# Kernel optimization log

Hardware: AMD Instinct MI355X
Metric: run time of the kernel (lower is better)

Reference implementation:

```python
import jax, jax.numpy as jnp
import numpy as np

B, N, K, IN = 8, 2048, 8, 5
BN = B * N

def _lin(k, i, o):
    s = 1.0 / np.sqrt(i)
    return jax.random.uniform(k, (i, o), jnp.float32, -s, s)

def setup_inputs() -> dict:
    key = jax.random.key(0)
    ks = jax.random.split(key, 12)
    inp = {"points": jax.random.normal(ks[0], (B, N, IN), jnp.float32)}
    dims = [(IN * 2, 64), (64 * 2, 128), (128 * 2, 256)]
    for n, (i, o) in enumerate(dims, 1):
        inp[f"W{n}"] = _lin(ks[n], i, o)
        inp[f"b{n}"] = jnp.zeros((o,), jnp.float32)
        inp[f"g{n}"] = jnp.ones((o,), jnp.float32)
        inp[f"be{n}"] = jnp.zeros((o,), jnp.float32)
    inp["Wf1"] = _lin(ks[10], 448, 512); inp["bf1"] = jnp.zeros((512,), jnp.float32)
    inp["gf"] = jnp.ones((512,), jnp.float32); inp["bef"] = jnp.zeros((512,), jnp.float32)
    inp["Wf2"] = _lin(ks[11], 512, 128); inp["bf2"] = jnp.zeros((128,), jnp.float32)
    return inp

def _lrelu(x):
    return jnp.where(x >= 0, x, 0.2 * x)

def _bn(x, g, b, eps=1e-5):
    # BatchNorm1d in training mode: per-feature batch statistics
    m = x.mean(0)
    v = x.var(0)
    return (x - m) * jax.lax.rsqrt(v + eps) * g + b

def _knn_idx(pos):
    # pos: [B,N,3] -> neighbor indices [B,N,K], self excluded
    sq = (pos * pos).sum(-1)
    d = sq[:, :, None] + sq[:, None, :] - 2.0 * jnp.einsum('bnc,bmc->bnm', pos, pos)
    d = d + jnp.eye(N, dtype=d.dtype) * 1e10  # exclude self
    _, idx = jax.lax.top_k(-d, K)
    return idx

def _edge_conv(x, src, dst, W, b, g, be):
    # PyG EdgeConv: msg = nn(cat[x_i, x_j - x_i]); aggr='max' at target i
    xc = x[dst]
    xn = x[src]
    h = jnp.concatenate([xc, xn - xc], axis=-1) @ W + b
    h = _bn(_lrelu(h), g, be)
    return jax.ops.segment_max(h, dst, num_segments=BN)

def reference(points, W1, b1, g1, be1, W2, b2, g2, be2, W3, b3, g3, be3,
              Wf1, bf1, gf, bef, Wf2, bf2):
    pos = points[..., :3]                      # [B,N,3]
    idx = _knn_idx(pos)                        # [B,N,K]
    offs = (jnp.arange(B) * N)[:, None, None]
    src = (idx + offs).reshape(-1)             # neighbor (source) node ids [E]
    dst = jnp.repeat(jnp.arange(BN), K)        # center (target) node ids [E]
    x = points.reshape(BN, IN)
    x1 = _edge_conv(x, src, dst, W1, b1, g1, be1)   # [BN,64]
    x2 = _edge_conv(x1, src, dst, W2, b2, g2, be2)  # [BN,128]
    x3 = _edge_conv(x2, src, dst, W3, b3, g3, be3)  # [BN,256]
    xs = jnp.concatenate([x1, x2, x3], axis=-1).reshape(B, N, 448)
    gfeat = xs.max(axis=1)                     # global max pool per cloud [B,448]
    h = _bn(_lrelu(gfeat @ Wf1 + bf1), gf, bef)
    return h @ Wf2 + bf2                       # [B,128]
```

## Files before the change

kernel.cpp:

```cpp
#include <hip/hip_runtime.h>
#include <math.h>

#define B_ 8
#define N_ 2048
#define K_ 8
#define IN_ 5
#define BN_ (B_*N_)
#define NEDGE_ (BN_*K_)
#define GRP 8
#define SEG_ 32
#define CSEG_ (N_/SEG_)
#define CHUNKS_ (N_/GRP)

typedef unsigned short ushort8_ __attribute__((ext_vector_type(8)));
typedef short bf16x8_ __attribute__((ext_vector_type(8)));
typedef float f32x4_ __attribute__((ext_vector_type(4)));

__device__ inline unsigned short f2bf(float f) {
    unsigned int u = __float_as_uint(f);
    u += 0x7fffu + ((u >> 16) & 1u);
    return (unsigned short)(u >> 16);
}
__device__ inline float bf2f(unsigned short h) {
    return __uint_as_float(((unsigned int)h) << 16);
}

__global__ __launch_bounds__(256) void knn_part(const float4* __restrict__ P4,
                                                unsigned long long* __restrict__ part) {
    int tid = threadIdx.x;
    int bblk = blockIdx.x >> 3;
    int q = blockIdx.x * 256 + tid;
    int nloc = q & (N_-1);
    int seg = blockIdx.y;

    float4 qp = P4[q];
    float qx2 = -2.0f*qp.x, qy2 = -2.0f*qp.y, qz2 = -2.0f*qp.z;
    float qsq = qp.w;

    unsigned int bd[K_], bi[K_];
#pragma unroll
    for (int k = 0; k < K_; ++k) { bd[k] = 0xFFFFFFFFu; bi[k] = 0xFFFFFFFFu; }

    const float4* __restrict__ cb = P4 + ((size_t)bblk << 11) + (size_t)seg*CSEG_;
    int jbase = seg * CSEG_;

#pragma unroll 8
    for (int jj = 0; jj < CSEG_; ++jj) {
        float4 c = cb[jj];
        float d = qsq + c.w;
        d = fmaf(qx2, c.x, d);
        d = fmaf(qy2, c.y, d);
        d = fmaf(qz2, c.z, d);
        unsigned int cd = __float_as_uint(d);
        int jg = jbase + jj;
        cd = (jg == nloc) ? 0xFFFFFFFFu : cd;
        unsigned int ci = (unsigned int)jg;
#pragma unroll
        for (int p = 0; p < K_; ++p) {
            bool lt = cd < bd[p];
            unsigned int nd = lt ? cd : bd[p];
            unsigned int xd = lt ? bd[p] : cd;
            unsigned int ni = lt ? ci : bi[p];
            unsigned int xi = lt ? bi[p] : ci;
            bd[p] = nd; cd = xd; bi[p] = ni; ci = xi;
        }
    }
    unsigned long long* op = part + ((size_t)seg * BN_ + q) * K_;
#pragma unroll
    for (int k = 0; k < K_; ++k)
        op[k] = ((unsigned long long)bd[k] << 32) | bi[k];
}

__global__ __launch_bounds__(128) void knn_merge(const unsigned long long* __restrict__ part,
                                                 int* __restrict__ src) {
    int q = blockIdx.x * 128 + threadIdx.x;
    int b = q / N_;
    unsigned long long best[K_];
#pragma unroll
    for (int k = 0; k < K_; ++k) best[k] = ~0ull;
    for (int s = 0; s < SEG_; ++s) {
        const unsigned long long* lp = part + ((size_t)s * BN_ + q) * K_;
#pragma unroll
        for (int k = 0; k < K_; ++k) {
            unsigned long long key = lp[k];
            if (key >= best[K_-1]) break;
            unsigned long long cur = key;
#pragma unroll
            for (int p = 0; p < K_; ++p) {
                unsigned long long lo = best[p] < cur ? best[p] : cur;
                unsigned long long hi = best[p] < cur ? cur : best[p];
                best[p] = lo; cur = hi;
            }
        }
    }
#pragma unroll
    for (int k = 0; k < K_; ++k)
        src[(size_t)q*K_ + k] = b*N_ + (int)(best[k] & 0xFFFFFFFFu);
}

__global__ __launch_bounds__(256) void cast_prep1(const float* __restrict__ X,
                                                  unsigned short* __restrict__ Xh,
                                                  unsigned short* __restrict__ Xl,
                                                  float4* __restrict__ P4,
                                                  const float* __restrict__ W1,
                                                  const float* __restrict__ b1,
                                                  unsigned short* __restrict__ WTh,
                                                  unsigned short* __restrict__ WTl,
                                                  float* __restrict__ cvec) {
    const int total8 = BN_ * 32 / 8;
    int t = blockIdx.x * 256 + threadIdx.x;
    if (t < total8) {
        int m = t >> 2;
        int k0 = (t & 3) * 8;
        ushort8_ vh, vl;
#pragma unroll
        for (int j = 0; j < 8; ++j) {
            int k = k0 + j;
            float v = (k < IN_) ? X[(size_t)m*IN_ + k] : 0.0f;
            unsigned short h = f2bf(v);
            vh[j] = h;
            vl[j] = f2bf(v - bf2f(h));
        }
        *(ushort8_*)(Xh + (size_t)m*32 + k0) = vh;
        *(ushort8_*)(Xl + (size_t)m*32 + k0) = vl;
        if (t < BN_) {
            const float* p = X + (size_t)t*IN_;
            float x = p[0], y = p[1], z = p[2];
            P4[t] = make_float4(x, y, z, x*x + y*y + z*z);
        }
    } else {
        int idx = t - total8;
        const int nWT = 2*64*32;
        if (idx < nWT) {
            int n = idx >> 5;
            int k = idx & 31;
            float val = 0.0f;
            if (k < IN_) {
                if (n < 64) val = W1[(size_t)k*64 + n] - W1[(size_t)(IN_+k)*64 + n];
                else        val = W1[(size_t)(IN_+k)*64 + (n - 64)];
            }
            unsigned short h = f2bf(val);
            WTh[(size_t)n*32 + k] = h;
            WTl[(size_t)n*32 + k] = f2bf(val - bf2f(h));
        } else if (idx < nWT + 64) {
            int c = idx - nWT;
            cvec[c] = b1[c];
        }
    }
}

__global__ __launch_bounds__(256) void prep_layer(const float* __restrict__ W,
                                                  const float* __restrict__ scale,
                                                  const float* __restrict__ shift,
                                                  const float* __restrict__ bias,
                                                  unsigned short* __restrict__ WTh,
                                                  unsigned short* __restrict__ WTl,
                                                  float* __restrict__ cvec,
                                                  int Cin, int C, int Kpad) {
    int idx = blockIdx.x * 256 + threadIdx.x;
    int nWT = 2*C*Kpad;
    if (idx < nWT) {
        int n = idx / Kpad;
        int k = idx % Kpad;
        float val = 0.0f;
        if (k < Cin) {
            float s = scale[k];
            if (n < C) val = s * (W[(size_t)k*C + n] - W[(size_t)(Cin+k)*C + n]);
            else       val = s * W[(size_t)(Cin+k)*C + (n - C)];
        }
        unsigned short h = f2bf(val);
        WTh[(size_t)n*Kpad + k] = h;
        WTl[(size_t)n*Kpad + k] = f2bf(val - bf2f(h));
    } else if (idx < nWT + C) {
        int c = idx - nWT;
        float acc = bias[c];
        for (int d = 0; d < Cin; ++d) acc += shift[d] * W[(size_t)d*C + c];
        cvec[c] = acc;
    }
}

__global__ __launch_bounds__(256) void mfma_dual(const unsigned short* __restrict__ Xh,
                                                 const unsigned short* __restrict__ Xl,
                                                 const unsigned short* __restrict__ WTh,
                                                 const unsigned short* __restrict__ WTl,
                                                 float* __restrict__ PQ, int K, int Ntot,
                                                 int gx) {
    __shared__ unsigned short sXh[128*32], sXl[128*32], sWh[128*32], sWl[128*32];
    int n = blockIdx.x;
    int by = (n & 7) + 8*(n/(8*gx));
    int bx = (n >> 3) % gx;
    int tid = threadIdx.x, l = tid & 63, w = tid >> 6;
    int wr = w >> 1, wc = w & 1;
    int bm = by * 128, bn0 = bx * 128;

    f32x4_ acc[4][4];
#pragma unroll
    for (int i = 0; i < 4; ++i)
#pragma unroll
        for (int j = 0; j < 4; ++j) acc[i][j] = (f32x4_){0.f, 0.f, 0.f, 0.f};

    for (int k0 = 0; k0 < K; k0 += 32) {
#pragma unroll
        for (int i = 0; i < 2; ++i) {
            int idx = tid + i*256;
            int row = idx >> 2;
            int col0 = (idx & 3) * 8;
            size_t gxo = (size_t)(bm  + row)*K + k0 + col0;
            size_t gwo = (size_t)(bn0 + row)*K + k0 + col0;
            int lo_ = ((row << 6) | (col0 << 1)) ^ ((row & 7) << 4);
            *(ushort8_*)((char*)sXh + lo_) = *(const ushort8_*)(Xh + gxo);
            *(ushort8_*)((char*)sXl + lo_) = *(const ushort8_*)(Xl + gxo);
            *(ushort8_*)((char*)sWh + lo_) = *(const ushort8_*)(WTh + gwo);
            *(ushort8_*)((char*)sWl + lo_) = *(const ushort8_*)(WTl + gwo);
        }
        __syncthreads();

        int kb = (l >> 4) << 4;
        bf16x8_ bh[4], bl4[4];
#pragma unroll
        for (int nf = 0; nf < 4; ++nf) {
            int rn = wc*64 + nf*16 + (l & 15);
            int o = ((rn << 6) | kb) ^ ((rn & 7) << 4);
            bh[nf]  = *(const bf16x8_*)((const char*)sWh + o);
            bl4[nf] = *(const bf16x8_*)((const char*)sWl + o);
        }
#pragma unroll
        for (int mf = 0; mf < 4; ++mf) {
            int rm = wr*64 + mf*16 + (l & 15);
            int o = ((rm << 6) | kb) ^ ((rm & 7) << 4);
            bf16x8_ ah = *(const bf16x8_*)((const char*)sXh + o);
            bf16x8_ al = *(const bf16x8_*)((const char*)sXl + o);
#pragma unroll
            for (int nf = 0; nf < 4; ++nf) {
                acc[mf][nf] = __builtin_amdgcn_mfma_f32_16x16x32_bf16(ah, bh[nf],  acc[mf][nf], 0, 0, 0);
                acc[mf][nf] = __builtin_amdgcn_mfma_f32_16x16x32_bf16(ah, bl4[nf], acc[mf][nf], 0, 0, 0);
                acc[mf][nf] = __builtin_amdgcn_mfma_f32_16x16x32_bf16(al, bh[nf],  acc[mf][nf], 0, 0, 0);
            }
        }
        __syncthreads();
    }

    int r0 = (l >> 4) << 2, cB = l & 15;
#pragma unroll
    for (int mf = 0; mf < 4; ++mf)
#pragma unroll
        for (int nf = 0; nf < 4; ++nf) {
            int col = bn0 + wc*64 + nf*16 + cB;
#pragma unroll
            for (int reg = 0; reg < 4; ++reg) {
                int row = bm + wr*64 + mf*16 + r0 + reg;
                PQ[(size_t)row*Ntot + col] = acc[mf][nf][reg];
            }
        }
}

__global__ void combine_kernel(const float* __restrict__ P, const float* __restrict__ Q,
                               const float* __restrict__ cvec, const int* __restrict__ src,
                               unsigned short* __restrict__ Xh_out, unsigned short* __restrict__ Xl_out,
                               float* __restrict__ partial, float* __restrict__ gpart,
                               int C, int S) {
    int pb = blockIdx.x;
    int lb = (pb & 7) * CHUNKS_ + (pb >> 3);
    int c = threadIdx.x;
    int i0 = lb * GRP;
    float cv = cvec[c];
    float sum = 0.f, ssq = 0.f;
    float bmx = -INFINITY;
    for (int g = 0; g < GRP; ++g) {
        int i = i0 + g;
        float p = P[(size_t)i*S + c] + cv;
        float mx = -INFINITY;
#pragma unroll
        for (int k = 0; k < K_; ++k) {
            int s = src[(size_t)i*K_ + k];
            float h = p + Q[(size_t)s*S + c];
            float l = (h >= 0.f) ? h : 0.2f*h;
            sum += l; ssq += l*l;
            mx = fmaxf(mx, l);
        }
        if (Xh_out) {
            unsigned short hh = f2bf(mx);
            Xh_out[(size_t)i*C + c] = hh;
            Xl_out[(size_t)i*C + c] = f2bf(mx - bf2f(hh));
        }
        bmx = fmaxf(bmx, mx);
    }
    gpart[(size_t)lb*C + c] = bmx;
    partial[(size_t)lb*2*C + c]     = sum;
    partial[(size_t)lb*2*C + C + c] = ssq;
}

__global__ __launch_bounds__(256) void reduce_kernel(const float* __restrict__ partial, int nblocks, int C,
                              const float* __restrict__ g, const float* __restrict__ be,
                              float* __restrict__ scale, float* __restrict__ shift) {
    int c = blockIdx.x;
    float s0 = 0.f, s1 = 0.f;
    for (int blk = threadIdx.x; blk < nblocks; blk += 256) {
        s0 += partial[(size_t)blk*2*C + c];
        s1 += partial[(size_t)blk*2*C + C + c];
    }
    __shared__ float l0[256], l1[256];
    l0[threadIdx.x] = s0; l1[threadIdx.x] = s1;
    __syncthreads();
    for (int off = 128; off > 0; off >>= 1) {
        if (threadIdx.x < off) {
            l0[threadIdx.x] += l0[threadIdx.x + off];
            l1[threadIdx.x] += l1[threadIdx.x + off];
        }
        __syncthreads();
    }
    if (threadIdx.x == 0) {
        float mean = l0[0] / (float)NEDGE_;
        float var  = l1[0] / (float)NEDGE_ - mean*mean;
        float sc = g[c] * rsqrtf(var + 1e-5f);
        scale[c] = sc;
        shift[c] = be[c] - mean*sc;
    }
}

__global__ __launch_bounds__(1024) void gmax_finalize(
        const float* __restrict__ gp1, const float* __restrict__ gp2, const float* __restrict__ gp3,
        const float* __restrict__ sc1, const float* __restrict__ sh1,
        const float* __restrict__ sc2, const float* __restrict__ sh2,
        const float* __restrict__ sc3, const float* __restrict__ sh3,
        float* __restrict__ gfeat) {
    int b = blockIdx.x, grp = blockIdx.y;
    const float *gp, *sc, *sh; int C, c0, coff;
    if (grp == 0)      { gp = gp1; sc = sc1; sh = sh1; C = 64;  c0 = 0;            coff = 0;   }
    else if (grp <= 2) { gp = gp2; sc = sc2; sh = sh2; C = 128; c0 = (grp-1)*64;   coff = 64;  }
    else               { gp = gp3; sc = sc3; sh = sh3; C = 256; c0 = (grp-3)*64;   coff = 192; }
    int cl = threadIdx.x & 63;
    int stripe = threadIdx.x >> 6;
    int c = c0 + cl;
    float mx = -INFINITY;
    for (int ch = stripe; ch < CHUNKS_; ch += 16)
        mx = fmaxf(mx, gp[((size_t)b*CHUNKS_ + ch)*C + c]);
    __shared__ float red[16][64];
    red[stripe][cl] = mx;
    __syncthreads();
    for (int off = 8; off > 0; off >>= 1) {
        if (stripe < off) red[stripe][cl] = fmaxf(red[stripe][cl], red[stripe+off][cl]);
        __syncthreads();
    }
    if (stripe == 0)
        gfeat[b*448 + coff + c] = sc[c]*red[0][cl] + sh[c];
}

__global__ __launch_bounds__(256) void final1(const float* __restrict__ gfeat,
                                              const float* __restrict__ Wf1, const float* __restrict__ bf1,
                                              const float* __restrict__ gf, const float* __restrict__ bef,
                                              float* __restrict__ H) {
    __shared__ float gfs[B_][448];
    __shared__ float red[4][64][B_];
    int t = threadIdx.x;
    int cl = t & 63;
    int stripe = t >> 6;
    int c = blockIdx.x * 64 + cl;
    for (int e = t; e < B_*448; e += 256) gfs[e/448][e%448] = gfeat[e];
    __syncthreads();
    float acc[B_] = {};
    for (int d = stripe*112; d < stripe*112 + 112; ++d) {
        float w = Wf1[(size_t)d*512 + c];
#pragma unroll
        for (int r = 0; r < B_; ++r) acc[r] += gfs[r][d] * w;
    }
#pragma unroll
    for (int r = 0; r < B_; ++r) red[stripe][cl][r] = acc[r];
    __syncthreads();
    if (stripe == 0) {
        float v[B_];
        float b1v = bf1[c];
#pragma unroll
        for (int r = 0; r < B_; ++r) {
            float a = red[0][cl][r] + red[1][cl][r] + red[2][cl][r] + red[3][cl][r] + b1v;
            v[r] = (a >= 0.f) ? a : 0.2f*a;
        }
        float mean = 0.f;
#pragma unroll
        for (int r = 0; r < B_; ++r) mean += v[r];
        mean *= (1.0f/B_);
        float var = 0.f;
#pragma unroll
        for (int r = 0; r < B_; ++r) { float dd = v[r] - mean; var += dd*dd; }
        var *= (1.0f/B_);
        float sc = gf[c] * rsqrtf(var + 1e-5f);
        float sh = bef[c] - mean*sc;
#pragma unroll
        for (int r = 0; r < B_; ++r) H[(size_t)r*512 + c] = v[r]*sc + sh;
    }
}

__global__ __launch_bounds__(128) void final2(const float* __restrict__ H,
                                              const float* __restrict__ Wf2, const float* __restrict__ bf2,
                                              float* __restrict__ out) {
    int b = blockIdx.x, c = threadIdx.x;
    __shared__ float hs[512];
    for (int e = c; e < 512; e += 128) hs[e] = H[(size_t)b*512 + e];
    __syncthreads();
    float a = bf2[c];
    for (int d = 0; d < 512; ++d) a += hs[d] * Wf2[(size_t)d*128 + c];
    out[b*128 + c] = a;
}

extern "C" void kernel_launch(void* const* d_in, const int* in_sizes, int n_in,
                              void* d_out, int out_size, void* d_ws, size_t ws_size,
                              hipStream_t stream) {
    (void)in_sizes; (void)n_in; (void)out_size; (void)ws_size;
    const float* points = (const float*)d_in[0];
    const float* W1 = (const float*)d_in[1];  const float* b1 = (const float*)d_in[2];
    const float* g1 = (const float*)d_in[3];  const float* be1 = (const float*)d_in[4];
    const float* W2 = (const float*)d_in[5];  const float* b2 = (const float*)d_in[6];
    const float* g2 = (const float*)d_in[7];  const float* be2 = (const float*)d_in[8];
    const float* W3 = (const float*)d_in[9];  const float* b3 = (const float*)d_in[10];
    const float* g3 = (const float*)d_in[11]; const float* be3 = (const float*)d_in[12];
    const float* Wf1 = (const float*)d_in[13]; const float* bf1 = (const float*)d_in[14];
    const float* gf = (const float*)d_in[15];  const float* bef = (const float*)d_in[16];
    const float* Wf2 = (const float*)d_in[17]; const float* bf2 = (const float*)d_in[18];
    float* out = (float*)d_out;

    size_t off = 0;
    char* base = (char*)d_ws;
    auto carve = [&](size_t bytes) -> void* {
        void* p = base + off;
        off += (bytes + 255) & ~(size_t)255;
        return p;
    };
    int*   src     = (int*)  carve((size_t)NEDGE_ * 4);
    float* PQ      = (float*)carve((size_t)BN_ * 512 * 4);
    float* gp1     = (float*)carve((size_t)(BN_/GRP) * 64 * 4);
    float* gp2     = (float*)carve((size_t)(BN_/GRP) * 128 * 4);
    float* gp3     = (float*)carve((size_t)(BN_/GRP) * 256 * 4);
    unsigned short* XhA = (unsigned short*)carve((size_t)BN_ * 128 * 2);
    unsigned short* XlA = (unsigned short*)carve((size_t)BN_ * 128 * 2);
    unsigned short* XhB = (unsigned short*)carve((size_t)BN_ * 128 * 2);
    unsigned short* XlB = (unsigned short*)carve((size_t)BN_ * 128 * 2);
    unsigned short* WTh = (unsigned short*)carve((size_t)512 * 128 * 2);
    unsigned short* WTl = (unsigned short*)carve((size_t)512 * 128 * 2);
    float4* P4     = (float4*)carve((size_t)BN_ * 16);
    float* cvec    = (float*)carve(256 * 4);
    float* sc1     = (float*)carve(64 * 4);
    float* sh1     = (float*)carve(64 * 4);
    float* sc2     = (float*)carve(128 * 4);
    float* sh2     = (float*)carve(128 * 4);
    float* sc3     = (float*)carve(256 * 4);
    float* sh3     = (float*)carve(256 * 4);
    float* partial = (float*)carve((size_t)(BN_/GRP) * 2 * 256 * 4);
    float* gfeat   = (float*)carve((size_t)B_ * 448 * 4);
    float* H       = (float*)carve((size_t)B_ * 512 * 4);

    cast_prep1<<<(65536 + 4096 + 64 + 255)/256, 256, 0, stream>>>(
        points, XhA, XlA, P4, W1, b1, WTh, WTl, cvec);

    unsigned long long* part = (unsigned long long*)PQ;
    knn_part<<<dim3(BN_/256, SEG_), 256, 0, stream>>>(P4, part);
    knn_merge<<<BN_/128, 128, 0, stream>>>(part, src);

    mfma_dual<<<1*(BN_/128), 256, 0, stream>>>(XhA, XlA, WTh, WTl, PQ, 32, 128, 1);
    combine_kernel<<<BN_/GRP, 64, 0, stream>>>(PQ, PQ + 64, cvec, src, XhB, XlB, partial, gp1, 64, 128);
    reduce_kernel<<<64, 256, 0, stream>>>(partial, BN_/GRP, 64, g1, be1, sc1, sh1);

    prep_layer<<<(2*128*64 + 128 + 255)/256, 256, 0, stream>>>(W2, sc1, sh1, b2, WTh, WTl, cvec, 64, 128, 64);
    mfma_dual<<<2*(BN_/128), 256, 0, stream>>>(XhB, XlB, WTh, WTl, PQ, 64, 256, 2);
    combine_kernel<<<BN_/GRP, 128, 0, stream>>>(PQ, PQ + 128, cvec, src, XhA, XlA, partial, gp2, 128, 256);
    reduce_kernel<<<128, 256, 0, stream>>>(partial, BN_/GRP, 128, g2, be2, sc2, sh2);

    prep_layer<<<(2*256*128 + 256 + 255)/256, 256, 0, stream>>>(W3, sc2, sh2, b3, WTh, WTl, cvec, 128, 256, 128);
    mfma_dual<<<4*(BN_/128), 256, 0, stream>>>(XhA, XlA, WTh, WTl, PQ, 128, 512, 4);
    combine_kernel<<<BN_/GRP, 256, 0, stream>>>(PQ, PQ + 256, cvec, src, nullptr, nullptr, partial, gp3, 256, 512);
    reduce_kernel<<<256, 256, 0, stream>>>(partial, BN_/GRP, 256, g3, be3, sc3, sh3);

    gmax_finalize<<<dim3(B_, 7), 1024, 0, stream>>>(gp1, gp2, gp3,
                                                    sc1, sh1, sc2, sh2, sc3, sh3, gfeat);

    final1<<<8, 256, 0, stream>>>(gfeat, Wf1, bf1, gf, bef, H);
    final2<<<8, 128, 0, stream>>>(H, Wf2, bf2, out);
}
```

Before: 219.6 us.

## Vectorize edge-combine kernels with float4 loads and 256-thread blocks

Replaces the scalar combine kernel (one thread per channel, 64-256 threads per block) with a templated version. Each thread handles four channels through float4 gathers, blocks always use 256 threads spanning several points, and neighbor indices are staged in shared memory. Per-block sum, sum-of-squares and max are reduced in shared memory before being written. Layer 1 now groups 16 points per block, and the gmax/partial buffer sizes and chunk counts are adjusted to match. The aim is fewer memory transactions and better occupancy, at the cost of an extra shared-memory reduction per block.

```diff
diff --git a/kernel.cpp b/kernel.cpp
--- a/kernel.cpp
+++ b/kernel.cpp
@@ -7,12 +7,11 @@
 #define IN_ 5
 #define BN_ (B_*N_)
 #define NEDGE_ (BN_*K_)
-#define GRP 8
 #define SEG_ 32
 #define CSEG_ (N_/SEG_)
-#define CHUNKS_ (N_/GRP)
 
 typedef unsigned short ushort8_ __attribute__((ext_vector_type(8)));
+typedef unsigned short ushort4_ __attribute__((ext_vector_type(4)));
 typedef short bf16x8_ __attribute__((ext_vector_type(8)));
 typedef float f32x4_ __attribute__((ext_vector_type(4)));
 
@@ -254,40 +253,85 @@
         }
 }
 
-__global__ void combine_kernel(const float* __restrict__ P, const float* __restrict__ Q,
-                               const float* __restrict__ cvec, const int* __restrict__ src,
-                               unsigned short* __restrict__ Xh_out, unsigned short* __restrict__ Xl_out,
-                               float* __restrict__ partial, float* __restrict__ gpart,
-                               int C, int S) {
+template<int C, int GRPL>
+__global__ __launch_bounds__(256) void combine_f4(
+        const float* __restrict__ P, const float* __restrict__ Q,
+        const float* __restrict__ cvec, const int* __restrict__ src,
+        unsigned short* __restrict__ Xh_out, unsigned short* __restrict__ Xl_out,
+        float* __restrict__ partial, float* __restrict__ gpart,
+        int S, int chunks) {
+    constexpr int VPC = C / 4;
+    constexpr int PPR = 256 / VPC;
+    constexpr int ROUNDS = GRPL / PPR;
+    constexpr int NS = GRPL * K_;
+
     int pb = blockIdx.x;
-    int lb = (pb & 7) * CHUNKS_ + (pb >> 3);
-    int c = threadIdx.x;
-    int i0 = lb * GRP;
-    float cv = cvec[c];
-    float sum = 0.f, ssq = 0.f;
-    float bmx = -INFINITY;
-    for (int g = 0; g < GRP; ++g) {
-        int i = i0 + g;
-        float p = P[(size_t)i*S + c] + cv;
-        float mx = -INFINITY;
+    int lb = (pb & 7) * chunks + (pb >> 3);
+    int tid = threadIdx.x;
+    int tc = tid & (VPC - 1);
+    int tq = tid / VPC;
+    int ch0 = tc * 4;
+    int i0 = lb * GRPL;
+
+    __shared__ int ssrc[NS];
+    if (tid < NS) ssrc[tid] = src[(size_t)i0 * K_ + tid];
+    __syncthreads();
+
+    f32x4_ cv = *(const f32x4_*)(cvec + ch0);
+    f32x4_ sum = (f32x4_){0.f,0.f,0.f,0.f};
+    f32x4_ ssq = (f32x4_){0.f,0.f,0.f,0.f};
+    f32x4_ bmx = (f32x4_){-INFINITY,-INFINITY,-INFINITY,-INFINITY};
+
+#pragma unroll
+    for (int r = 0; r < ROUNDS; ++r) {
+        int il = r * PPR + tq;
+        int i = i0 + il;
+        f32x4_ p = *(const f32x4_*)(P + (size_t)i*S + ch0) + cv;
+        f32x4_ mx = (f32x4_){-INFINITY,-INFINITY,-INFINITY,-INFINITY};
 #pragma unroll
         for (int k = 0; k < K_; ++k) {
-            int s = src[(size_t)i*K_ + k];
-            float h = p + Q[(size_t)s*S + c];
-            float l = (h >= 0.f) ? h : 0.2f*h;
-            sum += l; ssq += l*l;
-            mx = fmaxf(mx, l);
+            int s = ssrc[il*K_ + k];
+            f32x4_ q = *(const f32x4_*)(Q + (size_t)s*S + ch0);
+#pragma unroll
+            for (int j = 0; j < 4; ++j) {
+                float h = p[j] + q[j];
+                float l = (h >= 0.f) ? h : 0.2f*h;
+                sum[j] += l; ssq[j] += l*l;
+                mx[j] = fmaxf(mx[j], l);
+            }
         }
         if (Xh_out) {
-            unsigned short hh = f2bf(mx);
-            Xh_out[(size_t)i*C + c] = hh;
-            Xl_out[(size_t)i*C + c] = f2bf(mx - bf2f(hh));
-        }
-        bmx = fmaxf(bmx, mx);
-    }
-    gpart[(size_t)lb*C + c] = bmx;
-    partial[(size_t)lb*2*C + c]     = sum;
-    partial[(size_t)lb*2*C + C + c] = ssq;
+            ushort4_ hv, lv;
+#pragma unroll
+            for (int j = 0; j < 4; ++j) {
+                unsigned short hh = f2bf(mx[j]);
+                hv[j] = hh;
+                lv[j] = f2bf(mx[j] - bf2f(hh));
+            }
+            *(ushort4_*)(Xh_out + (size_t)i*C + ch0) = hv;
+            *(ushort4_*)(Xl_out + (size_t)i*C + ch0) = lv;
+        }
+#pragma unroll
+        for (int j = 0; j < 4; ++j) bmx[j] = fmaxf(bmx[j], mx[j]);
+    }
+
+    __shared__ f32x4_ f0[256], f1[256], f2[256];
+    f0[tid] = sum; f1[tid] = ssq; f2[tid] = bmx;
+    __syncthreads();
+    for (int off = 128; off >= VPC; off >>= 1) {
+        if (tid < off) {
+            f0[tid] += f0[tid + off];
+            f1[tid] += f1[tid + off];
+#pragma unroll
+            for (int j = 0; j < 4; ++j) f2[tid][j] = fmaxf(f2[tid][j], f2[tid + off][j]);
+        }
+        __syncthreads();
+    }
+    if (tid < VPC) {
+        *(f32x4_*)(gpart + (size_t)lb*C + ch0) = f2[tid];
+        *(f32x4_*)(partial + (size_t)lb*2*C + ch0)     = f0[tid];
+        *(f32x4_*)(partial + (size_t)lb*2*C + C + ch0) = f1[tid];
+    }
 }
 
 __global__ __launch_bounds__(256) void reduce_kernel(const float* __restrict__ partial, int nblocks, int C,
@@ -325,16 +369,16 @@
         const float* __restrict__ sc3, const float* __restrict__ sh3,
         float* __restrict__ gfeat) {
     int b = blockIdx.x, grp = blockIdx.y;
-    const float *gp, *sc, *sh; int C, c0, coff;
-    if (grp == 0)      { gp = gp1; sc = sc1; sh = sh1; C = 64;  c0 = 0;            coff = 0;   }
-    else if (grp <= 2) { gp = gp2; sc = sc2; sh = sh2; C = 128; c0 = (grp-1)*64;   coff = 64;  }
-    else               { gp = gp3; sc = sc3; sh = sh3; C = 256; c0 = (grp-3)*64;   coff = 192; }
+    const float *gp, *sc, *sh; int C, c0, coff, CH;
+    if (grp == 0)      { gp = gp1; sc = sc1; sh = sh1; C = 64;  c0 = 0;          coff = 0;   CH = 128; }
+    else if (grp <= 2) { gp = gp2; sc = sc2; sh = sh2; C = 128; c0 = (grp-1)*64; coff = 64;  CH = 256; }
+    else               { gp = gp3; sc = sc3; sh = sh3; C = 256; c0 = (grp-3)*64; coff = 192; CH = 256; }
     int cl = threadIdx.x & 63;
     int stripe = threadIdx.x >> 6;
     int c = c0 + cl;
     float mx = -INFINITY;
-    for (int ch = stripe; ch < CHUNKS_; ch += 16)
-        mx = fmaxf(mx, gp[((size_t)b*CHUNKS_ + ch)*C + c]);
+    for (int ch = stripe; ch < CH; ch += 16)
+        mx = fmaxf(mx, gp[((size_t)b*CH + ch)*C + c]);
     __shared__ float red[16][64];
     red[stripe][cl] = mx;
     __syncthreads();
@@ -427,9 +471,9 @@
     };
     int*   src     = (int*)  carve((size_t)NEDGE_ * 4);
     float* PQ      = (float*)carve((size_t)BN_ * 512 * 4);
-    float* gp1     = (float*)carve((size_t)(BN_/GRP) * 64 * 4);
-    float* gp2     = (float*)carve((size_t)(BN_/GRP) * 128 * 4);
-    float* gp3     = (float*)carve((size_t)(BN_/GRP) * 256 * 4);
+    float* gp1     = (float*)carve((size_t)(BN_/16) * 64 * 4);
+    float* gp2     = (float*)carve((size_t)(BN_/8) * 128 * 4);
+    float* gp3     = (float*)carve((size_t)(BN_/8) * 256 * 4);
     unsigned short* XhA = (unsigned short*)carve((size_t)BN_ * 128 * 2);
     unsigned short* XlA = (unsigned short*)carve((size_t)BN_ * 128 * 2);
     unsigned short* XhB = (unsigned short*)carve((size_t)BN_ * 128 * 2);
@@ -444,7 +488,7 @@
     float* sh2     = (float*)carve(128 * 4);
     float* sc3     = (float*)carve(256 * 4);
     float* sh3     = (float*)carve(256 * 4);
-    float* partial = (float*)carve((size_t)(BN_/GRP) * 2 * 256 * 4);
+    float* partial = (float*)carve((size_t)(BN_/8) * 2 * 256 * 4);
     float* gfeat   = (float*)carve((size_t)B_ * 448 * 4);
     float* H       = (float*)carve((size_t)B_ * 512 * 4);
 
@@ -456,18 +500,21 @@
     knn_merge<<<BN_/128, 128, 0, stream>>>(part, src);
 
     mfma_dual<<<1*(BN_/128), 256, 0, stream>>>(XhA, XlA, WTh, WTl, PQ, 32, 128, 1);
-    combine_kernel<<<BN_/GRP, 64, 0, stream>>>(PQ, PQ + 64, cvec, src, XhB, XlB, partial, gp1, 64, 128);
-    reduce_kernel<<<64, 256, 0, stream>>>(partial, BN_/GRP, 64, g1, be1, sc1, sh1);
+    combine_f4<64,16><<<BN_/16, 256, 0, stream>>>(PQ, PQ + 64, cvec, src, XhB, XlB,
+                                                  partial, gp1, 128, 128);
+    reduce_kernel<<<64, 256, 0, stream>>>(partial, BN_/16, 64, g1, be1, sc1, sh1);
 
     prep_layer<<<(2*128*64 + 128 + 255)/256, 256, 0, stream>>>(W2, sc1, sh1, b2, WTh, WTl, cvec, 64, 128, 64);
     mfma_dual<<<2*(BN_/128), 256, 0, stream>>>(XhB, XlB, WTh, WTl, PQ, 64, 256, 2);
-    combine_kernel<<<BN_/GRP, 128, 0, stream>>>(PQ, PQ + 128, cvec, src, XhA, XlA, partial, gp2, 128, 256);
-    reduce_kernel<<<128, 256, 0, stream>>>(partial, BN_/GRP, 128, g2, be2, sc2, sh2);
+    combine_f4<128,8><<<BN_/8, 256, 0, stream>>>(PQ, PQ + 128, cvec, src, XhA, XlA,
+                                                 partial, gp2, 256, 256);
+    reduce_kernel<<<128, 256, 0, stream>>>(partial, BN_/8, 128, g2, be2, sc2, sh2);
 
     prep_layer<<<(2*256*128 + 256 + 255)/256, 256, 0, stream>>>(W3, sc2, sh2, b3, WTh, WTl, cvec, 128, 256, 128);
     mfma_dual<<<4*(BN_/128), 256, 0, stream>>>(XhA, XlA, WTh, WTl, PQ, 128, 512, 4);
-    combine_kernel<<<BN_/GRP, 256, 0, stream>>>(PQ, PQ + 256, cvec, src, nullptr, nullptr, partial, gp3, 256, 512);
-    reduce_kernel<<<256, 256, 0, stream>>>(partial, BN_/GRP, 256, g3, be3, sc3, sh3);
+    combine_f4<256,8><<<BN_/8, 256, 0, stream>>>(PQ, PQ + 256, cvec, src, nullptr, nullptr,
+                                                 partial, gp3, 512, 256);
+    reduce_kernel<<<256, 256, 0, stream>>>(partial, BN_/8, 256, g3, be3, sc3, sh3);
 
     gmax_finalize<<<dim3(B_, 7), 1024, 0, stream>>>(gp1, gp2, gp3,
                                                     sc1, sh1, sc2, sh2, sc3, sh3, gfeat);
```

Result: faster. 214.2 us (median of 2 runs) (-2.5%).
